# Kernel optimization log

Hardware: AMD Instinct MI355X
Metric: run time of the kernel (lower is better)

## Reference

```python
import jax, jax.numpy as jnp
import numpy as np

B = 524288
H = 64  # hidden_dim
D = 1   # input_dim


def setup_inputs() -> dict:
    key = jax.random.key(0)
    ks = jax.random.split(key, 16)
    s = 0.05
    inp = {
        "gradients": jax.random.normal(ks[0], (B, D), jnp.float32),
        "parameters": jax.random.normal(ks[1], (B, D), jnp.float32),
        "momentum": jax.random.normal(ks[2], (B, D), jnp.float32),
        "h0": jax.random.normal(ks[3], (B, H), jnp.float32),
        "c0": jax.random.normal(ks[4], (B, H), jnp.float32),
        # input_processor: Linear(3D->H), ReLU, Linear(H->H)
        "W1": jax.random.normal(ks[5], (H, 3 * D), jnp.float32) * s,
        "b1": jax.random.normal(ks[6], (H,), jnp.float32) * s,
        "W2": jax.random.normal(ks[7], (H, H), jnp.float32) * s,
        "b2": jax.random.normal(ks[8], (H,), jnp.float32) * s,
        # LSTM cell (PyTorch layout: gates stacked i,f,g,o -> 4H rows)
        "W_ih": jax.random.normal(ks[9], (4 * H, H), jnp.float32) * s,
        "W_hh": jax.random.normal(ks[10], (4 * H, H), jnp.float32) * s,
        "b_ih": jax.random.normal(ks[11], (4 * H,), jnp.float32) * s,
        "b_hh": jax.random.normal(ks[12], (4 * H,), jnp.float32) * s,
        # output_layer: Linear(H->D)
        "W_out": jax.random.normal(ks[13], (D, H), jnp.float32) * s,
        "b_out": jax.random.normal(ks[14], (D,), jnp.float32) * s,
    }
    return inp


def reference(gradients, parameters, momentum, h0, c0,
              W1, b1, W2, b2, W_ih, W_hh, b_ih, b_hh, W_out, b_out):
    # momentum update
    m = 0.9 * momentum + gradients                      # [B, D]
    feats = jnp.concatenate([gradients, parameters, m], axis=-1)  # [B, 3D]
    # small MLP
    x = jax.nn.relu(feats @ W1.T + b1) @ W2.T + b2      # [B, H]
    # single-step LSTM cell, PyTorch gate order i, f, g, o
    gates = x @ W_ih.T + b_ih + h0 @ W_hh.T + b_hh      # [B, 4H]
    i, f, g, o = jnp.split(gates, 4, axis=-1)
    c1 = jax.nn.sigmoid(f) * c0 + jax.nn.sigmoid(i) * jnp.tanh(g)
    h1 = jax.nn.sigmoid(o) * jnp.tanh(c1)               # [B, H]
    update = h1 @ W_out.T + b_out                       # [B, D]
    return update
```

## Files before the change

kernel.cpp:

```cpp
#include <hip/hip_runtime.h>
#include <hip/hip_bf16.h>
#include <stdint.h>


typedef __attribute__((ext_vector_type(8))) __bf16  bf16x8;
typedef __attribute__((ext_vector_type(8))) float   f32x8;
typedef __attribute__((ext_vector_type(4))) float   floatx4;

__device__ __forceinline__ unsigned short f2bf_bits(float x){
    unsigned u = __builtin_bit_cast(unsigned, x);
    u = u + 0x7fffu + ((u >> 16) & 1u);
    return (unsigned short)(u >> 16);
}
__device__ __forceinline__ bf16x8 pack8(float4 a, float4 b){
    f32x8 t;
    t[0]=a.x; t[1]=a.y; t[2]=a.z; t[3]=a.w;
    t[4]=b.x; t[5]=b.y; t[6]=b.z; t[7]=b.w;
    return __builtin_convertvector(t, bf16x8);
}

__global__ __launch_bounds__(256) void prep_kernel(
    const float* __restrict__ W2, const float* __restrict__ b2,
    const float* __restrict__ W_ih, const float* __restrict__ W_hh,
    const float* __restrict__ b_ih, const float* __restrict__ b_hh,
    unsigned short* __restrict__ wc, float* __restrict__ biasc)
{
    __shared__ float W2s[64*64];
    __shared__ float b2s[64];
    __shared__ float wihs[16*64];
    const int tid = threadIdx.x;
    const int b   = blockIdx.x;

    for (int i = 0; i < 4; i++){
        int idx = i*1024 + tid*4;
        *(float4*)(W2s + idx) = *(const float4*)(W2 + idx);
    }
    if (tid < 64) b2s[tid] = b2[tid];
    {
        int idx = tid*4;
        *(float4*)(wihs + idx) = *(const float4*)(W_ih + b*16*64 + idx);
    }
    __syncthreads();

    const int nl = tid >> 4;
    const int n  = b*16 + nl;
    const int jg = tid & 15;
    const int j  = jg*4;
    const int T  = n >> 4;

    float a0=0.f, a1=0.f, a2=0.f, a3=0.f;
    for (int h = 0; h < 64; h++){
        float wv = wihs[nl*64 + h];
        const float* w2r = W2s + h*64 + j;
        a0 += wv*w2r[0]; a1 += wv*w2r[1]; a2 += wv*w2r[2]; a3 += wv*w2r[3];
    }
    auto store4 = [&](int k, float v0, float v1, float v2, float v3){
        int s    = k >> 5;
        int lane = ((k >> 3) & 3)*16 + (n & 15);
        int off  = (T*4 + s)*512 + lane*8 + (k & 7);
        ushort4 v; v.x=f2bf_bits(v0); v.y=f2bf_bits(v1); v.z=f2bf_bits(v2); v.w=f2bf_bits(v3);
        *(ushort4*)(wc + off) = v;
    };
    store4(j, a0, a1, a2, a3);
    {
        const float* src = W_hh + n*64 + j;
        store4(64 + j, src[0], src[1], src[2], src[3]);
    }
    if (jg == 0){
        float s = b_ih[n] + b_hh[n];
        for (int h = 0; h < 64; h++) s += wihs[nl*64 + h]*b2s[h];
        biasc[n] = s;
    }
}

__global__ __launch_bounds__(1024, 4) void main_kernel(
    const float* __restrict__ grad, const float* __restrict__ param,
    const float* __restrict__ mom,  const float* __restrict__ h0,
    const float* __restrict__ c0,   const float* __restrict__ W1,
    const float* __restrict__ b1,   const float* __restrict__ Wout,
    const float* __restrict__ bout,
    const unsigned short* __restrict__ wc, const float* __restrict__ biasc,
    float* __restrict__ out)
{
    __shared__ __align__(16) unsigned short wc_l[32768];
    __shared__ float  bias_l[256];
    __shared__ float4 w1p_l[64];
    __shared__ float  wout_l[64];

    const int tid  = threadIdx.x;
    const int lane = tid & 63;
    const int w    = tid >> 6;
    const int l15  = lane & 15;
    const int q    = lane >> 4;

    {
        const float4* src = (const float4*)wc;
        float4*       dst = (float4*)wc_l;
        #pragma unroll
        for (int i = 0; i < 4; i++)
            dst[i*1024 + tid] = src[i*1024 + tid];
    }
    if (tid < 256){
        float sc = ((tid >> 6) == 2) ? 2.885390082f : -1.442695041f;
        bias_l[tid] = sc * biasc[tid];
    } else if (tid < 320){
        int j = tid - 256;
        w1p_l[j] = make_float4(W1[j*3], W1[j*3+1], W1[j*3+2], b1[j]);
    } else if (tid < 384){
        wout_l[tid - 320] = Wout[tid - 320];
    }

    const float bout0 = bout[0];
    constexpr int NCH = 4;
    const long blockBase = (long)blockIdx.x * (NCH * 256);

    {
        long rA = blockBase + w*16 + l15;
    }
    long rA0 = blockBase + w*16 + l15;
    float g_r  = grad[rA0];
    float p_r  = param[rA0];
    float mo_r = mom[rA0];
    const float* hr0 = h0 + rA0*64;
    float4 ha = *(const float4*)(hr0 + q*8);
    float4 hb = *(const float4*)(hr0 + q*8 + 4);
    float4 hc = *(const float4*)(hr0 + 32 + q*8);
    float4 hd = *(const float4*)(hr0 + 32 + q*8 + 4);

    __syncthreads();

    const floatx4 zq = {0.f, 0.f, 0.f, 0.f};

    #pragma unroll 1
    for (int t = 0; t < NCH; ++t){
        const long rowt = blockBase + t*256;

        float m = fmaf(0.9f, mo_r, g_r);
        f32x8 rlo, rhi;
        #pragma unroll
        for (int jj = 0; jj < 8; jj++){
            float4 wr = w1p_l[q*8 + jj];
            float v = fmaf(wr.x, g_r, fmaf(wr.y, p_r, fmaf(wr.z, m, wr.w)));
            rlo[jj] = v > 0.f ? v : 0.f;
        }
        #pragma unroll
        for (int jj = 0; jj < 8; jj++){
            float4 wr = w1p_l[32 + q*8 + jj];
            float v = fmaf(wr.x, g_r, fmaf(wr.y, p_r, fmaf(wr.z, m, wr.w)));
            rhi[jj] = v > 0.f ? v : 0.f;
        }
        bf16x8 afr0 = __builtin_convertvector(rlo, bf16x8);
        bf16x8 afr1 = __builtin_convertvector(rhi, bf16x8);
        bf16x8 afr2 = pack8(ha, hb);
        bf16x8 afr3 = pack8(hc, hd);

        if (t != NCH-1){
            long rAn = rowt + 256 + w*16 + l15;
            g_r  = grad[rAn];
            p_r  = param[rAn];
            mo_r = mom[rAn];
            const float* hrn = h0 + rAn*64;
            ha = *(const float4*)(hrn + q*8);
            hb = *(const float4*)(hrn + q*8 + 4);
            hc = *(const float4*)(hrn + 32 + q*8);
            hd = *(const float4*)(hrn + 32 + q*8 + 4);
        }

        const float* c0b = c0 + (rowt + w*16 + q*4)*64 + l15;
        float red[4] = {0.f, 0.f, 0.f, 0.f};

        #pragma unroll 1
        for (int jh = 0; jh < 4; ++jh){
            const int jh16 = jh << 4;

            float c0v[4];
            c0v[0] = c0b[jh16];
            c0v[1] = c0b[jh16 + 64];
            c0v[2] = c0b[jh16 + 128];
            c0v[3] = c0b[jh16 + 192];

            float bsi = bias_l[jh16 + l15];
            float bsf = bias_l[jh16 + l15 + 64];
            float bsg = bias_l[jh16 + l15 + 128];
            float bso = bias_l[jh16 + l15 + 192];
            float wo  = wout_l[jh16 + l15];

            const unsigned short* cb = wc_l + jh*2048 + lane*8;
            #define BFRAG(o) (*(const bf16x8*)(cb + (o)))
            floatx4 xi, xf, xg, xo;
            xi = __builtin_amdgcn_mfma_f32_16x16x32_bf16(afr0, BFRAG(0),         zq, 0,0,0);
            xi = __builtin_amdgcn_mfma_f32_16x16x32_bf16(afr1, BFRAG(512),       xi, 0,0,0);
            xi = __builtin_amdgcn_mfma_f32_16x16x32_bf16(afr2, BFRAG(1024),      xi, 0,0,0);
            xi = __builtin_amdgcn_mfma_f32_16x16x32_bf16(afr3, BFRAG(1536),      xi, 0,0,0);
            xf = __builtin_amdgcn_mfma_f32_16x16x32_bf16(afr0, BFRAG(8192),      zq, 0,0,0);
            xf = __builtin_amdgcn_mfma_f32_16x16x32_bf16(afr1, BFRAG(8192+512),  xf, 0,0,0);
            xf = __builtin_amdgcn_mfma_f32_16x16x32_bf16(afr2, BFRAG(8192+1024), xf, 0,0,0);
            xf = __builtin_amdgcn_mfma_f32_16x16x32_bf16(afr3, BFRAG(8192+1536), xf, 0,0,0);
            xg = __builtin_amdgcn_mfma_f32_16x16x32_bf16(afr0, BFRAG(16384),     zq, 0,0,0);
            xg = __builtin_amdgcn_mfma_f32_16x16x32_bf16(afr1, BFRAG(16384+512), xg, 0,0,0);
            xg = __builtin_amdgcn_mfma_f32_16x16x32_bf16(afr2, BFRAG(16384+1024),xg, 0,0,0);
            xg = __builtin_amdgcn_mfma_f32_16x16x32_bf16(afr3, BFRAG(16384+1536),xg, 0,0,0);
            xo = __builtin_amdgcn_mfma_f32_16x16x32_bf16(afr0, BFRAG(24576),     zq, 0,0,0);
            xo = __builtin_amdgcn_mfma_f32_16x16x32_bf16(afr1, BFRAG(24576+512), xo, 0,0,0);
            xo = __builtin_amdgcn_mfma_f32_16x16x32_bf16(afr2, BFRAG(24576+1024),xo, 0,0,0);
            xo = __builtin_amdgcn_mfma_f32_16x16x32_bf16(afr3, BFRAG(24576+1536),xo, 0,0,0);
            #undef BFRAG

            #pragma unroll
            for (int r = 0; r < 4; ++r){
                float ei = __builtin_amdgcn_exp2f(fmaf(-1.442695041f, xi[r], bsi));
                float iv = __builtin_amdgcn_rcpf(1.0f + ei);
                float ef = __builtin_amdgcn_exp2f(fmaf(-1.442695041f, xf[r], bsf));
                float fv = __builtin_amdgcn_rcpf(1.0f + ef);
                float eo = __builtin_amdgcn_exp2f(fmaf(-1.442695041f, xo[r], bso));
                float ov = __builtin_amdgcn_rcpf(1.0f + eo);
                float eg = __builtin_amdgcn_exp2f(fmaf( 2.885390082f, xg[r], bsg));
                float gv = fmaf(-2.0f, __builtin_amdgcn_rcpf(1.0f + eg), 1.0f);
                float c1 = fmaf(fv, c0v[r], iv*gv);
                float ec = __builtin_amdgcn_exp2f(2.885390082f * c1);
                float tv = fmaf(-2.0f, __builtin_amdgcn_rcpf(1.0f + ec), 1.0f);
                float h1 = ov * tv;
                red[r] = fmaf(h1, wo, red[r]);
            }
        }

        #pragma unroll
        for (int mset = 1; mset < 16; mset <<= 1)
            #pragma unroll
            for (int r = 0; r < 4; r++)
                red[r] += __shfl_xor(red[r], mset, 64);

        if (l15 == 0){
            long orow = rowt + w*16 + q*4;
            #pragma unroll
            for (int r = 0; r < 4; r++)
                out[orow + r] = red[r] + bout0;
        }
    }
}

extern "C" void kernel_launch(void* const* d_in, const int* in_sizes, int n_in,
                              void* d_out, int out_size, void* d_ws, size_t ws_size,
                              hipStream_t stream)
{
    const float* grad  = (const float*)d_in[0];
    const float* param = (const float*)d_in[1];
    const float* mom   = (const float*)d_in[2];
    const float* h0    = (const float*)d_in[3];
    const float* c0    = (const float*)d_in[4];
    const float* W1    = (const float*)d_in[5];
    const float* b1    = (const float*)d_in[6];
    const float* W2    = (const float*)d_in[7];
    const float* b2    = (const float*)d_in[8];
    const float* W_ih  = (const float*)d_in[9];
    const float* W_hh  = (const float*)d_in[10];
    const float* b_ih  = (const float*)d_in[11];
    const float* b_hh  = (const float*)d_in[12];
    const float* Wout  = (const float*)d_in[13];
    const float* bout  = (const float*)d_in[14];

    unsigned short* wc = (unsigned short*)d_ws;
    float* biasc       = (float*)((char*)d_ws + 65536);

    prep_kernel<<<16, 256, 0, stream>>>(W2, b2, W_ih, W_hh, b_ih, b_hh, wc, biasc);

    const int nblocks = 524288 / (4 * 256);
    main_kernel<<<nblocks, 1024, 0, stream>>>(grad, param, mom, h0, c0,
                                              W1, b1, Wout, bout, wc, biasc,
                                              (float*)d_out);
}
```

Measured before the change: 339.6 us.

## Process two row tiles per wave to reuse B fragments, drop chunk loop

Each wave now computes two 16-row tiles at once, loading each LDS weight fragment once and feeding it to two MFMAs. Blocks shrink to 512 threads handling 256 rows each, with no multi-chunk loop and no software prefetch, so 2048 blocks each stage the 64KB weight table into LDS. This halves LDS weight reads per row and adds MFMA ILP, but puts more pressure on registers, and the weight-staging cost per row goes up because each block covers fewer rows.

```diff
diff --git a/kernel.cpp b/kernel.cpp
--- a/kernel.cpp
+++ b/kernel.cpp
@@ -73,7 +73,7 @@
     }
 }
 
-__global__ __launch_bounds__(1024, 4) void main_kernel(
+__global__ __launch_bounds__(512, 4) void main_kernel(
     const float* __restrict__ grad, const float* __restrict__ param,
     const float* __restrict__ mom,  const float* __restrict__ h0,
     const float* __restrict__ c0,   const float* __restrict__ W1,
@@ -92,13 +92,14 @@
     const int w    = tid >> 6;
     const int l15  = lane & 15;
     const int q    = lane >> 4;
+    const long row0 = (long)blockIdx.x * 256;
 
     {
         const float4* src = (const float4*)wc;
         float4*       dst = (float4*)wc_l;
         #pragma unroll
-        for (int i = 0; i < 4; i++)
-            dst[i*1024 + tid] = src[i*1024 + tid];
+        for (int i = 0; i < 8; i++)
+            dst[i*512 + tid] = src[i*512 + tid];
     }
     if (tid < 256){
         float sc = ((tid >> 6) == 2) ? 2.885390082f : -1.442695041f;
@@ -110,131 +111,146 @@
         wout_l[tid - 320] = Wout[tid - 320];
     }
 
+    const long rA0 = row0 + w*32 + l15;
+    const long rA1 = rA0 + 16;
+    float g0 = grad[rA0], p0 = param[rA0], mo0 = mom[rA0];
+    float g1 = grad[rA1], p1 = param[rA1], mo1 = mom[rA1];
+    const float* hr0 = h0 + rA0*64;
+    float4 ha0 = *(const float4*)(hr0 + q*8);
+    float4 hb0 = *(const float4*)(hr0 + q*8 + 4);
+    float4 hc0 = *(const float4*)(hr0 + 32 + q*8);
+    float4 hd0 = *(const float4*)(hr0 + 32 + q*8 + 4);
+    const float* hr1 = h0 + rA1*64;
+    float4 ha1 = *(const float4*)(hr1 + q*8);
+    float4 hb1 = *(const float4*)(hr1 + q*8 + 4);
+    float4 hc1 = *(const float4*)(hr1 + 32 + q*8);
+    float4 hd1 = *(const float4*)(hr1 + 32 + q*8 + 4);
     const float bout0 = bout[0];
-    constexpr int NCH = 4;
-    const long blockBase = (long)blockIdx.x * (NCH * 256);
-
-    {
-        long rA = blockBase + w*16 + l15;
-    }
-    long rA0 = blockBase + w*16 + l15;
-    float g_r  = grad[rA0];
-    float p_r  = param[rA0];
-    float mo_r = mom[rA0];
-    const float* hr0 = h0 + rA0*64;
-    float4 ha = *(const float4*)(hr0 + q*8);
-    float4 hb = *(const float4*)(hr0 + q*8 + 4);
-    float4 hc = *(const float4*)(hr0 + 32 + q*8);
-    float4 hd = *(const float4*)(hr0 + 32 + q*8 + 4);
 
     __syncthreads();
 
+    float m0 = fmaf(0.9f, mo0, g0);
+    float m1 = fmaf(0.9f, mo1, g1);
+    f32x8 rlo0, rhi0, rlo1, rhi1;
+    #pragma unroll
+    for (int jj = 0; jj < 8; jj++){
+        float4 wr = w1p_l[q*8 + jj];
+        float v0 = fmaf(wr.x, g0, fmaf(wr.y, p0, fmaf(wr.z, m0, wr.w)));
+        float v1 = fmaf(wr.x, g1, fmaf(wr.y, p1, fmaf(wr.z, m1, wr.w)));
+        rlo0[jj] = v0 > 0.f ? v0 : 0.f;
+        rlo1[jj] = v1 > 0.f ? v1 : 0.f;
+    }
+    #pragma unroll
+    for (int jj = 0; jj < 8; jj++){
+        float4 wr = w1p_l[32 + q*8 + jj];
+        float v0 = fmaf(wr.x, g0, fmaf(wr.y, p0, fmaf(wr.z, m0, wr.w)));
+        float v1 = fmaf(wr.x, g1, fmaf(wr.y, p1, fmaf(wr.z, m1, wr.w)));
+        rhi0[jj] = v0 > 0.f ? v0 : 0.f;
+        rhi1[jj] = v1 > 0.f ? v1 : 0.f;
+    }
+    bf16x8 a0_0 = __builtin_convertvector(rlo0, bf16x8);
+    bf16x8 a1_0 = __builtin_convertvector(rhi0, bf16x8);
+    bf16x8 a2_0 = pack8(ha0, hb0);
+    bf16x8 a3_0 = pack8(hc0, hd0);
+    bf16x8 a0_1 = __builtin_convertvector(rlo1, bf16x8);
+    bf16x8 a1_1 = __builtin_convertvector(rhi1, bf16x8);
+    bf16x8 a2_1 = pack8(ha1, hb1);
+    bf16x8 a3_1 = pack8(hc1, hd1);
+
+    const float* c0b0 = c0 + (row0 + w*32 + q*4)*64 + l15;
+    const float* c0b1 = c0 + (row0 + w*32 + 16 + q*4)*64 + l15;
+
+    float red0[4] = {0.f, 0.f, 0.f, 0.f};
+    float red1[4] = {0.f, 0.f, 0.f, 0.f};
     const floatx4 zq = {0.f, 0.f, 0.f, 0.f};
 
     #pragma unroll 1
-    for (int t = 0; t < NCH; ++t){
-        const long rowt = blockBase + t*256;
-
-        float m = fmaf(0.9f, mo_r, g_r);
-        f32x8 rlo, rhi;
-        #pragma unroll
-        for (int jj = 0; jj < 8; jj++){
-            float4 wr = w1p_l[q*8 + jj];
-            float v = fmaf(wr.x, g_r, fmaf(wr.y, p_r, fmaf(wr.z, m, wr.w)));
-            rlo[jj] = v > 0.f ? v : 0.f;
-        }
-        #pragma unroll
-        for (int jj = 0; jj < 8; jj++){
-            float4 wr = w1p_l[32 + q*8 + jj];
-            float v = fmaf(wr.x, g_r, fmaf(wr.y, p_r, fmaf(wr.z, m, wr.w)));
-            rhi[jj] = v > 0.f ? v : 0.f;
-        }
-        bf16x8 afr0 = __builtin_convertvector(rlo, bf16x8);
-        bf16x8 afr1 = __builtin_convertvector(rhi, bf16x8);
-        bf16x8 afr2 = pack8(ha, hb);
-        bf16x8 afr3 = pack8(hc, hd);
-
-        if (t != NCH-1){
-            long rAn = rowt + 256 + w*16 + l15;
-            g_r  = grad[rAn];
-            p_r  = param[rAn];
-            mo_r = mom[rAn];
-            const float* hrn = h0 + rAn*64;
-            ha = *(const float4*)(hrn + q*8);
-            hb = *(const float4*)(hrn + q*8 + 4);
-            hc = *(const float4*)(hrn + 32 + q*8);
-            hd = *(const float4*)(hrn + 32 + q*8 + 4);
-        }
-
-        const float* c0b = c0 + (rowt + w*16 + q*4)*64 + l15;
-        float red[4] = {0.f, 0.f, 0.f, 0.f};
-
-        #pragma unroll 1
-        for (int jh = 0; jh < 4; ++jh){
-            const int jh16 = jh << 4;
-
-            float c0v[4];
-            c0v[0] = c0b[jh16];
-            c0v[1] = c0b[jh16 + 64];
-            c0v[2] = c0b[jh16 + 128];
-            c0v[3] = c0b[jh16 + 192];
-
-            float bsi = bias_l[jh16 + l15];
-            float bsf = bias_l[jh16 + l15 + 64];
-            float bsg = bias_l[jh16 + l15 + 128];
-            float bso = bias_l[jh16 + l15 + 192];
-            float wo  = wout_l[jh16 + l15];
-
-            const unsigned short* cb = wc_l + jh*2048 + lane*8;
-            #define BFRAG(o) (*(const bf16x8*)(cb + (o)))
-            floatx4 xi, xf, xg, xo;
-            xi = __builtin_amdgcn_mfma_f32_16x16x32_bf16(afr0, BFRAG(0),         zq, 0,0,0);
-            xi = __builtin_amdgcn_mfma_f32_16x16x32_bf16(afr1, BFRAG(512),       xi, 0,0,0);
-            xi = __builtin_amdgcn_mfma_f32_16x16x32_bf16(afr2, BFRAG(1024),      xi, 0,0,0);
-            xi = __builtin_amdgcn_mfma_f32_16x16x32_bf16(afr3, BFRAG(1536),      xi, 0,0,0);
-            xf = __builtin_amdgcn_mfma_f32_16x16x32_bf16(afr0, BFRAG(8192),      zq, 0,0,0);
-            xf = __builtin_amdgcn_mfma_f32_16x16x32_bf16(afr1, BFRAG(8192+512),  xf, 0,0,0);
-            xf = __builtin_amdgcn_mfma_f32_16x16x32_bf16(afr2, BFRAG(8192+1024), xf, 0,0,0);
-            xf = __builtin_amdgcn_mfma_f32_16x16x32_bf16(afr3, BFRAG(8192+1536), xf, 0,0,0);
-            xg = __builtin_amdgcn_mfma_f32_16x16x32_bf16(afr0, BFRAG(16384),     zq, 0,0,0);
-            xg = __builtin_amdgcn_mfma_f32_16x16x32_bf16(afr1, BFRAG(16384+512), xg, 0,0,0);
-            xg = __builtin_amdgcn_mfma_f32_16x16x32_bf16(afr2, BFRAG(16384+1024),xg, 0,0,0);
-            xg = __builtin_amdgcn_mfma_f32_16x16x32_bf16(afr3, BFRAG(16384+1536),xg, 0,0,0);
-            xo = __builtin_amdgcn_mfma_f32_16x16x32_bf16(afr0, BFRAG(24576),     zq, 0,0,0);
-            xo = __builtin_amdgcn_mfma_f32_16x16x32_bf16(afr1, BFRAG(24576+512), xo, 0,0,0);
-            xo = __builtin_amdgcn_mfma_f32_16x16x32_bf16(afr2, BFRAG(24576+1024),xo, 0,0,0);
-            xo = __builtin_amdgcn_mfma_f32_16x16x32_bf16(afr3, BFRAG(24576+1536),xo, 0,0,0);
-            #undef BFRAG
-
-            #pragma unroll
-            for (int r = 0; r < 4; ++r){
-                float ei = __builtin_amdgcn_exp2f(fmaf(-1.442695041f, xi[r], bsi));
-                float iv = __builtin_amdgcn_rcpf(1.0f + ei);
-                float ef = __builtin_amdgcn_exp2f(fmaf(-1.442695041f, xf[r], bsf));
-                float fv = __builtin_amdgcn_rcpf(1.0f + ef);
-                float eo = __builtin_amdgcn_exp2f(fmaf(-1.442695041f, xo[r], bso));
-                float ov = __builtin_amdgcn_rcpf(1.0f + eo);
-                float eg = __builtin_amdgcn_exp2f(fmaf( 2.885390082f, xg[r], bsg));
-                float gv = fmaf(-2.0f, __builtin_amdgcn_rcpf(1.0f + eg), 1.0f);
-                float c1 = fmaf(fv, c0v[r], iv*gv);
-                float ec = __builtin_amdgcn_exp2f(2.885390082f * c1);
-                float tv = fmaf(-2.0f, __builtin_amdgcn_rcpf(1.0f + ec), 1.0f);
-                float h1 = ov * tv;
-                red[r] = fmaf(h1, wo, red[r]);
-            }
-        }
-
-        #pragma unroll
-        for (int mset = 1; mset < 16; mset <<= 1)
-            #pragma unroll
-            for (int r = 0; r < 4; r++)
-                red[r] += __shfl_xor(red[r], mset, 64);
-
-        if (l15 == 0){
-            long orow = rowt + w*16 + q*4;
-            #pragma unroll
-            for (int r = 0; r < 4; r++)
-                out[orow + r] = red[r] + bout0;
+    for (int jh = 0; jh < 4; ++jh){
+        const int jh16 = jh << 4;
+
+        float c00[4], c01[4];
+        #pragma unroll
+        for (int r = 0; r < 4; ++r){
+            c00[r] = c0b0[jh16 + r*64];
+            c01[r] = c0b1[jh16 + r*64];
+        }
+
+        float bsi = bias_l[jh16 + l15];
+        float bsf = bias_l[jh16 + l15 + 64];
+        float bsg = bias_l[jh16 + l15 + 128];
+        float bso = bias_l[jh16 + l15 + 192];
+        float wo  = wout_l[jh16 + l15];
+
+        const unsigned short* cb = wc_l + jh*2048 + lane*8;
+        floatx4 xi0, xi1, xf0, xf1, xg0, xg1, xo0, xo1;
+
+        #define GATE(Gofs, d0, d1)                                            \
+        {                                                                     \
+            bf16x8 t0 = *(const bf16x8*)(cb + (Gofs));                        \
+            bf16x8 t1 = *(const bf16x8*)(cb + (Gofs) + 512);                  \
+            bf16x8 t2 = *(const bf16x8*)(cb + (Gofs) + 1024);                 \
+            bf16x8 t3 = *(const bf16x8*)(cb + (Gofs) + 1536);                 \
+            d0 = __builtin_amdgcn_mfma_f32_16x16x32_bf16(a0_0, t0, zq, 0,0,0);\
+            d1 = __builtin_amdgcn_mfma_f32_16x16x32_bf16(a0_1, t0, zq, 0,0,0);\
+            d0 = __builtin_amdgcn_mfma_f32_16x16x32_bf16(a1_0, t1, d0, 0,0,0);\
+            d1 = __builtin_amdgcn_mfma_f32_16x16x32_bf16(a1_1, t1, d1, 0,0,0);\
+            d0 = __builtin_amdgcn_mfma_f32_16x16x32_bf16(a2_0, t2, d0, 0,0,0);\
+            d1 = __builtin_amdgcn_mfma_f32_16x16x32_bf16(a2_1, t2, d1, 0,0,0);\
+            d0 = __builtin_amdgcn_mfma_f32_16x16x32_bf16(a3_0, t3, d0, 0,0,0);\
+            d1 = __builtin_amdgcn_mfma_f32_16x16x32_bf16(a3_1, t3, d1, 0,0,0);\
+        }
+        GATE(0,     xi0, xi1)
+        GATE(8192,  xf0, xf1)
+        GATE(16384, xg0, xg1)
+        GATE(24576, xo0, xo1)
+        #undef GATE
+
+        #pragma unroll
+        for (int r = 0; r < 4; ++r){
+            float ei = __builtin_amdgcn_exp2f(fmaf(-1.442695041f, xi0[r], bsi));
+            float iv = __builtin_amdgcn_rcpf(1.0f + ei);
+            float ef = __builtin_amdgcn_exp2f(fmaf(-1.442695041f, xf0[r], bsf));
+            float fv = __builtin_amdgcn_rcpf(1.0f + ef);
+            float eo = __builtin_amdgcn_exp2f(fmaf(-1.442695041f, xo0[r], bso));
+            float ov = __builtin_amdgcn_rcpf(1.0f + eo);
+            float eg = __builtin_amdgcn_exp2f(fmaf( 2.885390082f, xg0[r], bsg));
+            float gv = fmaf(-2.0f, __builtin_amdgcn_rcpf(1.0f + eg), 1.0f);
+            float c1 = fmaf(fv, c00[r], iv*gv);
+            float ec = __builtin_amdgcn_exp2f(2.885390082f * c1);
+            float tv = fmaf(-2.0f, __builtin_amdgcn_rcpf(1.0f + ec), 1.0f);
+            red0[r] = fmaf(ov * tv, wo, red0[r]);
+        }
+        #pragma unroll
+        for (int r = 0; r < 4; ++r){
+            float ei = __builtin_amdgcn_exp2f(fmaf(-1.442695041f, xi1[r], bsi));
+            float iv = __builtin_amdgcn_rcpf(1.0f + ei);
+            float ef = __builtin_amdgcn_exp2f(fmaf(-1.442695041f, xf1[r], bsf));
+            float fv = __builtin_amdgcn_rcpf(1.0f + ef);
+            float eo = __builtin_amdgcn_exp2f(fmaf(-1.442695041f, xo1[r], bso));
+            float ov = __builtin_amdgcn_rcpf(1.0f + eo);
+            float eg = __builtin_amdgcn_exp2f(fmaf( 2.885390082f, xg1[r], bsg));
+            float gv = fmaf(-2.0f, __builtin_amdgcn_rcpf(1.0f + eg), 1.0f);
+            float c1 = fmaf(fv, c01[r], iv*gv);
+            float ec = __builtin_amdgcn_exp2f(2.885390082f * c1);
+            float tv = fmaf(-2.0f, __builtin_amdgcn_rcpf(1.0f + ec), 1.0f);
+            red1[r] = fmaf(ov * tv, wo, red1[r]);
+        }
+    }
+
+    #pragma unroll
+    for (int mset = 1; mset < 16; mset <<= 1)
+        #pragma unroll
+        for (int r = 0; r < 4; r++){
+            red0[r] += __shfl_xor(red0[r], mset, 64);
+            red1[r] += __shfl_xor(red1[r], mset, 64);
+        }
+
+    if (l15 == 0){
+        long orow0 = row0 + w*32 + q*4;
+        #pragma unroll
+        for (int r = 0; r < 4; r++){
+            out[orow0 + r]      = red0[r] + bout0;
+            out[orow0 + 16 + r] = red1[r] + bout0;
         }
     }
 }
@@ -264,8 +280,8 @@
 
     prep_kernel<<<16, 256, 0, stream>>>(W2, b2, W_ih, W_hh, b_ih, b_hh, wc, biasc);
 
-    const int nblocks = 524288 / (4 * 256);
-    main_kernel<<<nblocks, 1024, 0, stream>>>(grad, param, mom, h0, c0,
-                                              W1, b1, Wout, bout, wc, biasc,
-                                              (float*)d_out);
-}
+    const int nblocks = 524288 / 256;
+    main_kernel<<<nblocks, 512, 0, stream>>>(grad, param, mom, h0, c0,
+                                             W1, b1, Wout, bout, wc, biasc,
+                                             (float*)d_out);
+}
```

Result: faster. 314.1 us (-7.5%).
